# Performance work log

Hardware: AMD Instinct MI355X
Metric: run time of the kernel (lower is better)

Reference implementation:

```python
import jax, jax.numpy as jnp
import numpy as np

B, S, E, H = 8, 2048, 1024, 64

def setup_inputs() -> dict:
    key = jax.random.key(0)
    k1, k2, k3, k4 = jax.random.split(key, 4)
    scale = 0.02
    return {
        "x": jax.random.normal(k1, (B, S, E), dtype=jnp.float32),
        "Wq": jax.random.normal(k2, (E, H), dtype=jnp.float32) * scale,
        "Wk": jax.random.normal(k3, (E, H), dtype=jnp.float32) * scale,
        "Wv": jax.random.normal(k4, (E, H), dtype=jnp.float32) * scale,
    }

def reference(x, Wq, Wk, Wv):
    # x: [B, S, E]; projections to [B, S, H]
    q = jnp.einsum("bse,eh->bsh", x, Wq)
    k = jnp.einsum("bse,eh->bsh", x, Wk)
    v = jnp.einsum("bse,eh->bsh", x, Wv)
    head_size = Wq.shape[1]
    # NOTE: original divides by head_size (not sqrt(head_size))
    scores = jnp.einsum("bqh,bkh->bqk", q, k) / head_size  # [B, S, S]
    seq = q.shape[1]
    causal = jnp.tril(jnp.ones((seq, seq), dtype=bool))
    scores = jnp.where(causal, scores, -jnp.inf)
    attn = jax.nn.softmax(scores, axis=-1)
    # dropout p=0.0 (eval) -> identity
    return jnp.einsum("bqk,bkh->bqh", attn, v)
```

## Files before the change

kernel.cpp:

```cpp
#include <hip/hip_runtime.h>


typedef __bf16 bf16;
typedef bf16 bf16x8 __attribute__((ext_vector_type(8)));
typedef bf16 bf16x4 __attribute__((ext_vector_type(4)));
typedef float v4f __attribute__((ext_vector_type(4)));

#define MFMA_BF16 __builtin_amdgcn_mfma_f32_16x16x32_bf16

constexpr int SEQ = 2048, EDIM = 1024, HDIM = 64;
constexpr float SCALE_L2E = 1.4426950408889634f / 64.0f;

__global__ __launch_bounds__(256) void prep_w_kernel(
    const float* __restrict__ Wq, const float* __restrict__ Wk,
    const float* __restrict__ Wv, bf16* __restrict__ Wt) {
  int mat = blockIdx.x >> 5, kseg = blockIdx.x & 31;
  const float* src = mat == 0 ? Wq : (mat == 1 ? Wk : Wv);
  int n = threadIdx.x & 63;
  int k0 = kseg * 32 + (threadIdx.x >> 6) * 8;
  bf16x8 v;
#pragma unroll
  for (int j = 0; j < 8; ++j)
    v[j] = (bf16)src[(k0 + j) * 64 + n];
  *reinterpret_cast<bf16x8*>(Wt + (size_t)(mat * 64 + n) * EDIM + k0) = v;
}

__global__ __launch_bounds__(256) void proj_kernel(
    const float* __restrict__ x, const bf16* __restrict__ Wt,
    bf16* __restrict__ qw, bf16* __restrict__ kw, bf16* __restrict__ vT) {
  __shared__ __align__(16) bf16 As[2][32][72];
  __shared__ __align__(16) bf16 Bs[2][192][72];

  const int t = threadIdx.x;
  const int m0 = blockIdx.x * 32;
  const int wv = t >> 6, lane = t & 63, quad = lane >> 4, l16 = lane & 15;

  v4f acc[2][3] = {};
  float4 aReg[2];
  bf16x8 bReg[6];

  auto loadA = [&](int kk) {
#pragma unroll
    for (int p = 0; p < 2; ++p) {
      int flat = p * 1024 + t * 4;
      int r = flat >> 6, c = flat & 63;
      aReg[p] = *reinterpret_cast<const float4*>(
          x + (size_t)(m0 + r) * EDIM + kk * 64 + c);
    }
  };
  auto loadB = [&](int kk) {
#pragma unroll
    for (int p = 0; p < 6; ++p) {
      int idx = p * 256 + t;
      int r = idx >> 3, off = (idx & 7) * 8;
      bReg[p] = *reinterpret_cast<const bf16x8*>(
          Wt + (size_t)r * EDIM + kk * 64 + off);
    }
  };

  loadA(0);
  loadB(0);

  for (int kk = 0; kk < 16; ++kk) {
    const int buf = kk & 1;
#pragma unroll
    for (int p = 0; p < 2; ++p) {
      int flat = p * 1024 + t * 4;
      int r = flat >> 6, c = flat & 63;
      bf16x4 h4 = {(bf16)aReg[p].x, (bf16)aReg[p].y,
                   (bf16)aReg[p].z, (bf16)aReg[p].w};
      *reinterpret_cast<bf16x4*>(&As[buf][r][c]) = h4;
    }
#pragma unroll
    for (int p = 0; p < 6; ++p) {
      int idx = p * 256 + t;
      int r = idx >> 3, off = (idx & 7) * 8;
      *reinterpret_cast<bf16x8*>(&Bs[buf][r][off]) = bReg[p];
    }
    __syncthreads();
    if (kk < 15) {
      loadA(kk + 1);
      loadB(kk + 1);
    }
#pragma unroll
    for (int ks = 0; ks < 2; ++ks) {
      bf16x8 af[2], bfr[3];
#pragma unroll
      for (int mi = 0; mi < 2; ++mi)
        af[mi] = *reinterpret_cast<const bf16x8*>(
            &As[buf][16 * mi + l16][32 * ks + 8 * quad]);
#pragma unroll
      for (int ni = 0; ni < 3; ++ni)
        bfr[ni] = *reinterpret_cast<const bf16x8*>(
            &Bs[buf][48 * wv + 16 * ni + l16][32 * ks + 8 * quad]);
#pragma unroll
      for (int mi = 0; mi < 2; ++mi)
#pragma unroll
        for (int ni = 0; ni < 3; ++ni)
          acc[mi][ni] = MFMA_BF16(af[mi], bfr[ni], acc[mi][ni], 0, 0, 0);
    }
  }

#pragma unroll
  for (int mi = 0; mi < 2; ++mi) {
    const int token0 = m0 + 16 * mi + 4 * quad;
#pragma unroll
    for (int ni = 0; ni < 3; ++ni) {
      int n = 48 * wv + 16 * ni + l16;
      if (n < 64) {
#pragma unroll
        for (int r = 0; r < 4; ++r)
          qw[(size_t)(token0 + r) * HDIM + n] = (bf16)acc[mi][ni][r];
      } else if (n < 128) {
#pragma unroll
        for (int r = 0; r < 4; ++r)
          kw[(size_t)(token0 + r) * HDIM + (n - 64)] = (bf16)acc[mi][ni][r];
      } else {
        int b = token0 >> 11, s0 = token0 & 2047;
        bf16x4 pk = {(bf16)acc[mi][ni][0], (bf16)acc[mi][ni][1],
                     (bf16)acc[mi][ni][2], (bf16)acc[mi][ni][3]};
        *reinterpret_cast<bf16x4*>(
            vT + ((size_t)(b * 64 + (n - 128))) * SEQ + s0) = pk;
      }
    }
  }
}

__global__ __launch_bounds__(256) void attn_kernel(
    const bf16* __restrict__ qw, const bf16* __restrict__ kw,
    const bf16* __restrict__ vT, float* __restrict__ out) {
  const int batch = blockIdx.x & 7;
  const int j = blockIdx.x >> 3;
  const int w = threadIdx.x >> 6;
  const int lane = threadIdx.x & 63;
  const int quad = lane >> 4, l16 = lane & 15;

  __shared__ __align__(16) bf16 p_lds[4][16][40];
  __shared__ __align__(16) float o_lds[3][16][68];
  __shared__ float l_lds[3][16];

  const bf16* qB = qw + (size_t)batch * SEQ * HDIM;
  const bf16* kB = kw + (size_t)batch * SEQ * HDIM;
  const bf16* vB = vT + (size_t)batch * HDIM * SEQ;

  const int q0 = j * 16;
  const int T = (j >> 1) + 1;

  const bf16* qp = qB + (size_t)(q0 + l16) * HDIM + quad * 8;
  bf16x8 aq0 = *reinterpret_cast<const bf16x8*>(qp);
  bf16x8 aq1 = *reinterpret_cast<const bf16x8*>(qp + 32);

  float l_part[4] = {0.f, 0.f, 0.f, 0.f};
  v4f accO[4] = {};

  for (int jt = w; jt < T; jt += 4) {
    const int k0 = jt * 32;
    v4f sAcc[2] = {};
#pragma unroll
    for (int nt = 0; nt < 2; ++nt) {
      const bf16* kp = kB + (size_t)(k0 + 16 * nt + l16) * HDIM + quad * 8;
      bf16x8 b0 = *reinterpret_cast<const bf16x8*>(kp);
      bf16x8 b1 = *reinterpret_cast<const bf16x8*>(kp + 32);
      sAcc[nt] = MFMA_BF16(aq0, b0, sAcc[nt], 0, 0, 0);
      sAcc[nt] = MFMA_BF16(aq1, b1, sAcc[nt], 0, 0, 0);
    }
    float pv[2][4];
#pragma unroll
    for (int nt = 0; nt < 2; ++nt)
#pragma unroll
      for (int r = 0; r < 4; ++r)
        pv[nt][r] = __builtin_amdgcn_exp2f(sAcc[nt][r] * SCALE_L2E);
    if (jt == T - 1) {
#pragma unroll
      for (int nt = 0; nt < 2; ++nt)
#pragma unroll
        for (int r = 0; r < 4; ++r)
          if (k0 + 16 * nt + l16 > q0 + 4 * quad + r) pv[nt][r] = 0.f;
    }
#pragma unroll
    for (int r = 0; r < 4; ++r) l_part[r] += pv[0][r] + pv[1][r];

#pragma unroll
    for (int nt = 0; nt < 2; ++nt)
#pragma unroll
      for (int r = 0; r < 4; ++r)
        p_lds[w][4 * quad + r][16 * nt + l16] = (bf16)pv[nt][r];
    asm volatile("s_waitcnt lgkmcnt(0)" ::: "memory");
    bf16x8 pa = *reinterpret_cast<const bf16x8*>(&p_lds[w][l16][8 * quad]);
#pragma unroll
    for (int nt = 0; nt < 4; ++nt) {
      bf16x8 bv = *reinterpret_cast<const bf16x8*>(
          vB + (size_t)(16 * nt + l16) * SEQ + k0 + 8 * quad);
      accO[nt] = MFMA_BF16(pa, bv, accO[nt], 0, 0, 0);
    }
  }

#pragma unroll
  for (int r = 0; r < 4; ++r) {
    float s = l_part[r];
    s += __shfl_xor(s, 1, 16);
    s += __shfl_xor(s, 2, 16);
    s += __shfl_xor(s, 4, 16);
    s += __shfl_xor(s, 8, 16);
    l_part[r] = s;
  }

  if (w > 0) {
#pragma unroll
    for (int nt = 0; nt < 4; ++nt)
#pragma unroll
      for (int r = 0; r < 4; ++r)
        o_lds[w - 1][4 * quad + r][16 * nt + l16] = accO[nt][r];
    if (l16 == 0) {
#pragma unroll
      for (int r = 0; r < 4; ++r) l_lds[w - 1][4 * quad + r] = l_part[r];
    }
  }
  __syncthreads();
  if (w == 0) {
#pragma unroll
    for (int r = 0; r < 4; ++r) {
      const int row = 4 * quad + r;
      float lt = l_part[r] + l_lds[0][row] + l_lds[1][row] + l_lds[2][row];
      float inv = 1.0f / lt;
      float* op = out + ((size_t)batch * SEQ + q0 + row) * HDIM;
#pragma unroll
      for (int nt = 0; nt < 4; ++nt)
        op[16 * nt + l16] =
            (accO[nt][r] + o_lds[0][row][16 * nt + l16] +
             o_lds[1][row][16 * nt + l16] + o_lds[2][row][16 * nt + l16]) *
            inv;
    }
  }
}

extern "C" void kernel_launch(void* const* d_in, const int* in_sizes, int n_in,
                              void* d_out, int out_size, void* d_ws,
                              size_t ws_size, hipStream_t stream) {
  const float* x = (const float*)d_in[0];
  const float* Wq = (const float*)d_in[1];
  const float* Wk = (const float*)d_in[2];
  const float* Wv = (const float*)d_in[3];

  char* ws = (char*)d_ws;
  bf16* Wt = (bf16*)(ws);
  bf16* qw = (bf16*)(ws + 0x60000);
  bf16* kw = (bf16*)(ws + 0x260000);
  bf16* vT = (bf16*)(ws + 0x460000);

  prep_w_kernel<<<96, 256, 0, stream>>>(Wq, Wk, Wv, Wt);
  proj_kernel<<<512, 256, 0, stream>>>(x, Wt, qw, kw, vT);
  attn_kernel<<<1024, 256, 0, stream>>>(qw, kw, vT, (float*)d_out);
}
```

Baseline: 150.0 us.

## Enlarge attention tiles to 32x64, pair causal blocks, and software-pipeline QK with PV

The attention kernel now processes 32 query rows per tile against 64-key tiles, so each K and V fragment load feeds twice as many MFMAs. Each block handles a mirrored pair of query tiles (j and 63-j) to balance the causal triangle, and the grid shrinks from 1024 to 256 blocks. Within each wave, the next tile's K load and QK/exp stage overlap the current PV MFMAs through a double-buffered P buffer in LDS. The trade-off is larger register and LDS use and fewer blocks, which may reduce occupancy and latency hiding.

```diff
diff --git a/kernel.cpp b/kernel.cpp
--- a/kernel.cpp
+++ b/kernel.cpp
@@ -130,106 +130,153 @@
     const bf16* __restrict__ qw, const bf16* __restrict__ kw,
     const bf16* __restrict__ vT, float* __restrict__ out) {
   const int batch = blockIdx.x & 7;
-  const int j = blockIdx.x >> 3;
+  const int pi = blockIdx.x >> 3;
   const int w = threadIdx.x >> 6;
   const int lane = threadIdx.x & 63;
   const int quad = lane >> 4, l16 = lane & 15;
 
-  __shared__ __align__(16) bf16 p_lds[4][16][40];
-  __shared__ __align__(16) float o_lds[3][16][68];
-  __shared__ float l_lds[3][16];
+  __shared__ __align__(16) bf16 p_lds[4][2][32][68];
+  __shared__ __align__(16) float o_lds[3][32][68];
+  __shared__ float l_lds[3][32];
 
   const bf16* qB = qw + (size_t)batch * SEQ * HDIM;
   const bf16* kB = kw + (size_t)batch * SEQ * HDIM;
   const bf16* vB = vT + (size_t)batch * HDIM * SEQ;
 
-  const int q0 = j * 16;
-  const int T = (j >> 1) + 1;
-
-  const bf16* qp = qB + (size_t)(q0 + l16) * HDIM + quad * 8;
-  bf16x8 aq0 = *reinterpret_cast<const bf16x8*>(qp);
-  bf16x8 aq1 = *reinterpret_cast<const bf16x8*>(qp + 32);
-
-  float l_part[4] = {0.f, 0.f, 0.f, 0.f};
-  v4f accO[4] = {};
-
-  for (int jt = w; jt < T; jt += 4) {
-    const int k0 = jt * 32;
-    v4f sAcc[2] = {};
-#pragma unroll
-    for (int nt = 0; nt < 2; ++nt) {
-      const bf16* kp = kB + (size_t)(k0 + 16 * nt + l16) * HDIM + quad * 8;
-      bf16x8 b0 = *reinterpret_cast<const bf16x8*>(kp);
-      bf16x8 b1 = *reinterpret_cast<const bf16x8*>(kp + 32);
-      sAcc[nt] = MFMA_BF16(aq0, b0, sAcc[nt], 0, 0, 0);
-      sAcc[nt] = MFMA_BF16(aq1, b1, sAcc[nt], 0, 0, 0);
-    }
-    float pv[2][4];
-#pragma unroll
-    for (int nt = 0; nt < 2; ++nt)
-#pragma unroll
-      for (int r = 0; r < 4; ++r)
-        pv[nt][r] = __builtin_amdgcn_exp2f(sAcc[nt][r] * SCALE_L2E);
-    if (jt == T - 1) {
-#pragma unroll
-      for (int nt = 0; nt < 2; ++nt)
-#pragma unroll
-        for (int r = 0; r < 4; ++r)
-          if (k0 + 16 * nt + l16 > q0 + 4 * quad + r) pv[nt][r] = 0.f;
-    }
-#pragma unroll
-    for (int r = 0; r < 4; ++r) l_part[r] += pv[0][r] + pv[1][r];
-
-#pragma unroll
-    for (int nt = 0; nt < 2; ++nt)
-#pragma unroll
-      for (int r = 0; r < 4; ++r)
-        p_lds[w][4 * quad + r][16 * nt + l16] = (bf16)pv[nt][r];
-    asm volatile("s_waitcnt lgkmcnt(0)" ::: "memory");
-    bf16x8 pa = *reinterpret_cast<const bf16x8*>(&p_lds[w][l16][8 * quad]);
-#pragma unroll
-    for (int nt = 0; nt < 4; ++nt) {
-      bf16x8 bv = *reinterpret_cast<const bf16x8*>(
-          vB + (size_t)(16 * nt + l16) * SEQ + k0 + 8 * quad);
-      accO[nt] = MFMA_BF16(pa, bv, accO[nt], 0, 0, 0);
-    }
-  }
-
-#pragma unroll
-  for (int r = 0; r < 4; ++r) {
-    float s = l_part[r];
-    s += __shfl_xor(s, 1, 16);
-    s += __shfl_xor(s, 2, 16);
-    s += __shfl_xor(s, 4, 16);
-    s += __shfl_xor(s, 8, 16);
-    l_part[r] = s;
-  }
-
-  if (w > 0) {
-#pragma unroll
-    for (int nt = 0; nt < 4; ++nt)
-#pragma unroll
-      for (int r = 0; r < 4; ++r)
-        o_lds[w - 1][4 * quad + r][16 * nt + l16] = accO[nt][r];
-    if (l16 == 0) {
-#pragma unroll
-      for (int r = 0; r < 4; ++r) l_lds[w - 1][4 * quad + r] = l_part[r];
-    }
-  }
-  __syncthreads();
-  if (w == 0) {
-#pragma unroll
-    for (int r = 0; r < 4; ++r) {
-      const int row = 4 * quad + r;
-      float lt = l_part[r] + l_lds[0][row] + l_lds[1][row] + l_lds[2][row];
-      float inv = 1.0f / lt;
-      float* op = out + ((size_t)batch * SEQ + q0 + row) * HDIM;
+  for (int sp = 0; sp < 2; ++sp) {
+    const int j = sp ? (63 - pi) : pi;
+    const int q0 = 32 * j;
+    const int T64 = (j + 2) >> 1;
+    const int nw = (T64 > w) ? (((T64 - 1 - w) >> 2) + 1) : 0;
+
+    bf16x8 aq[2][2];
+#pragma unroll
+    for (int mi = 0; mi < 2; ++mi)
+#pragma unroll
+      for (int kf = 0; kf < 2; ++kf)
+        aq[mi][kf] = *reinterpret_cast<const bf16x8*>(
+            qB + (size_t)(q0 + 16 * mi + l16) * HDIM + 32 * kf + 8 * quad);
+
+    v4f accO[2][4] = {};
+    float l_part[2][4] = {{0.f, 0.f, 0.f, 0.f}, {0.f, 0.f, 0.f, 0.f}};
+    bf16x8 kfr[4][2];
+
+    auto loadK = [&](int jt) {
 #pragma unroll
       for (int nt = 0; nt < 4; ++nt)
-        op[16 * nt + l16] =
-            (accO[nt][r] + o_lds[0][row][16 * nt + l16] +
-             o_lds[1][row][16 * nt + l16] + o_lds[2][row][16 * nt + l16]) *
-            inv;
+#pragma unroll
+        for (int kf = 0; kf < 2; ++kf)
+          kfr[nt][kf] = *reinterpret_cast<const bf16x8*>(
+              kB + (size_t)(64 * jt + 16 * nt + l16) * HDIM + 32 * kf +
+              8 * quad);
+    };
+    auto qk_exp_stage = [&](int jt, int slot) {
+      v4f s[2][4] = {};
+#pragma unroll
+      for (int mi = 0; mi < 2; ++mi)
+#pragma unroll
+        for (int nt = 0; nt < 4; ++nt) {
+          s[mi][nt] = MFMA_BF16(aq[mi][0], kfr[nt][0], s[mi][nt], 0, 0, 0);
+          s[mi][nt] = MFMA_BF16(aq[mi][1], kfr[nt][1], s[mi][nt], 0, 0, 0);
+        }
+      const bool last = (jt == T64 - 1);
+#pragma unroll
+      for (int mi = 0; mi < 2; ++mi)
+#pragma unroll
+        for (int nt = 0; nt < 4; ++nt)
+#pragma unroll
+          for (int r = 0; r < 4; ++r) {
+            float p = __builtin_amdgcn_exp2f(s[mi][nt][r] * SCALE_L2E);
+            if (last &&
+                (64 * jt + 16 * nt + l16 > q0 + 16 * mi + 4 * quad + r))
+              p = 0.f;
+            l_part[mi][r] += p;
+            p_lds[w][slot][16 * mi + 4 * quad + r][16 * nt + l16] = (bf16)p;
+          }
+    };
+
+    if (nw > 0) {
+      loadK(w);
+      qk_exp_stage(w, 0);
+    }
+    for (int i = 0; i < nw; ++i) {
+      const int jt = w + 4 * i;
+      const int k0 = 64 * jt;
+      if (i + 1 < nw) loadK(jt + 4);
+      bf16x8 vfr[4][2];
+#pragma unroll
+      for (int nt = 0; nt < 4; ++nt)
+#pragma unroll
+        for (int kc = 0; kc < 2; ++kc)
+          vfr[nt][kc] = *reinterpret_cast<const bf16x8*>(
+              vB + (size_t)(16 * nt + l16) * SEQ + k0 + 32 * kc + 8 * quad);
+      asm volatile("s_waitcnt lgkmcnt(0)" ::: "memory");
+      bf16x8 pa[2][2];
+#pragma unroll
+      for (int mi = 0; mi < 2; ++mi)
+#pragma unroll
+        for (int kc = 0; kc < 2; ++kc)
+          pa[mi][kc] = *reinterpret_cast<const bf16x8*>(
+              &p_lds[w][i & 1][16 * mi + l16][32 * kc + 8 * quad]);
+      if (i + 1 < nw) qk_exp_stage(jt + 4, (i + 1) & 1);
+#pragma unroll
+      for (int mi = 0; mi < 2; ++mi)
+#pragma unroll
+        for (int nt = 0; nt < 4; ++nt) {
+          accO[mi][nt] = MFMA_BF16(pa[mi][0], vfr[nt][0], accO[mi][nt], 0, 0, 0);
+          accO[mi][nt] = MFMA_BF16(pa[mi][1], vfr[nt][1], accO[mi][nt], 0, 0, 0);
+        }
+    }
+
+#pragma unroll
+    for (int mi = 0; mi < 2; ++mi)
+#pragma unroll
+      for (int r = 0; r < 4; ++r) {
+        float s = l_part[mi][r];
+        s += __shfl_xor(s, 1, 16);
+        s += __shfl_xor(s, 2, 16);
+        s += __shfl_xor(s, 4, 16);
+        s += __shfl_xor(s, 8, 16);
+        l_part[mi][r] = s;
+      }
+
+    __syncthreads();
+    if (w > 0) {
+#pragma unroll
+      for (int mi = 0; mi < 2; ++mi)
+#pragma unroll
+        for (int nt = 0; nt < 4; ++nt)
+#pragma unroll
+          for (int r = 0; r < 4; ++r)
+            o_lds[w - 1][16 * mi + 4 * quad + r][16 * nt + l16] =
+                accO[mi][nt][r];
+      if (l16 == 0) {
+#pragma unroll
+        for (int mi = 0; mi < 2; ++mi)
+#pragma unroll
+          for (int r = 0; r < 4; ++r)
+            l_lds[w - 1][16 * mi + 4 * quad + r] = l_part[mi][r];
+      }
+    }
+    __syncthreads();
+    if (w == 0) {
+#pragma unroll
+      for (int mi = 0; mi < 2; ++mi)
+#pragma unroll
+        for (int r = 0; r < 4; ++r) {
+          const int row = 16 * mi + 4 * quad + r;
+          float lt = l_part[mi][r] + l_lds[0][row] + l_lds[1][row] +
+                     l_lds[2][row];
+          float inv = 1.0f / lt;
+          float* op = out + ((size_t)batch * SEQ + q0 + row) * HDIM;
+#pragma unroll
+          for (int nt = 0; nt < 4; ++nt)
+            op[16 * nt + l16] =
+                (accO[mi][nt][r] + o_lds[0][row][16 * nt + l16] +
+                 o_lds[1][row][16 * nt + l16] +
+                 o_lds[2][row][16 * nt + l16]) *
+                inv;
+        }
     }
   }
 }
@@ -250,5 +297,5 @@
 
   prep_w_kernel<<<96, 256, 0, stream>>>(Wq, Wk, Wv, Wt);
   proj_kernel<<<512, 256, 0, stream>>>(x, Wt, qw, kw, vT);
-  attn_kernel<<<1024, 256, 0, stream>>>(qw, kw, vT, (float*)d_out);
+  attn_kernel<<<256, 256, 0, stream>>>(qw, kw, vT, (float*)d_out);
 }
```

After: 136.4 us. 9.1% less time.

## Pipeline projection and attention loads, pair causal query tiles per block

Applied to the files above, without the earlier changes.

The projection kernel stops staging W in shared memory. Each wave now loads its W fragments straight into registers, double-buffered, and A is prefetched two steps ahead. The attention kernel processes 64-key tiles with software-pipelined K loads and QK/exp overlapped with PV, and each block handles a short and a long causal query tile (j and 127-j) to balance work across half as many blocks. This aims to hide global memory latency and even out causal load imbalance, at the cost of more registers and an added barrier per iteration.

```diff
diff --git a/kernel.cpp b/kernel.cpp
--- a/kernel.cpp
+++ b/kernel.cpp
@@ -29,76 +29,67 @@
     const float* __restrict__ x, const bf16* __restrict__ Wt,
     bf16* __restrict__ qw, bf16* __restrict__ kw, bf16* __restrict__ vT) {
   __shared__ __align__(16) bf16 As[2][32][72];
-  __shared__ __align__(16) bf16 Bs[2][192][72];
 
   const int t = threadIdx.x;
   const int m0 = blockIdx.x * 32;
   const int wv = t >> 6, lane = t & 63, quad = lane >> 4, l16 = lane & 15;
+  const int ar = t >> 3, ac = (t & 7) * 8;
 
   v4f acc[2][3] = {};
-  float4 aReg[2];
-  bf16x8 bReg[6];
-
-  auto loadA = [&](int kk) {
-#pragma unroll
-    for (int p = 0; p < 2; ++p) {
-      int flat = p * 1024 + t * 4;
-      int r = flat >> 6, c = flat & 63;
-      aReg[p] = *reinterpret_cast<const float4*>(
-          x + (size_t)(m0 + r) * EDIM + kk * 64 + c);
-    }
+  float4 aReg[2][2];
+  bf16x8 bReg[2][6];
+
+  auto loadA = [&](int kk, int slot) {
+    const float* p = x + (size_t)(m0 + ar) * EDIM + kk * 64 + ac;
+    aReg[slot][0] = *reinterpret_cast<const float4*>(p);
+    aReg[slot][1] = *reinterpret_cast<const float4*>(p + 4);
   };
-  auto loadB = [&](int kk) {
-#pragma unroll
-    for (int p = 0; p < 6; ++p) {
-      int idx = p * 256 + t;
-      int r = idx >> 3, off = (idx & 7) * 8;
-      bReg[p] = *reinterpret_cast<const bf16x8*>(
-          Wt + (size_t)r * EDIM + kk * 64 + off);
-    }
+  auto loadB = [&](int kk, int slot) {
+#pragma unroll
+    for (int ks = 0; ks < 2; ++ks)
+#pragma unroll
+      for (int ni = 0; ni < 3; ++ni)
+        bReg[slot][ks * 3 + ni] = *reinterpret_cast<const bf16x8*>(
+            Wt + (size_t)(48 * wv + 16 * ni + l16) * EDIM + kk * 64 +
+            32 * ks + 8 * quad);
   };
 
-  loadA(0);
-  loadB(0);
-
+  loadA(0, 0);
+  loadA(1, 1);
+  loadB(0, 0);
+
+#pragma unroll 2
   for (int kk = 0; kk < 16; ++kk) {
     const int buf = kk & 1;
-#pragma unroll
-    for (int p = 0; p < 2; ++p) {
-      int flat = p * 1024 + t * 4;
-      int r = flat >> 6, c = flat & 63;
-      bf16x4 h4 = {(bf16)aReg[p].x, (bf16)aReg[p].y,
-                   (bf16)aReg[p].z, (bf16)aReg[p].w};
-      *reinterpret_cast<bf16x4*>(&As[buf][r][c]) = h4;
-    }
-#pragma unroll
-    for (int p = 0; p < 6; ++p) {
-      int idx = p * 256 + t;
-      int r = idx >> 3, off = (idx & 7) * 8;
-      *reinterpret_cast<bf16x8*>(&Bs[buf][r][off]) = bReg[p];
-    }
-    __syncthreads();
-    if (kk < 15) {
-      loadA(kk + 1);
-      loadB(kk + 1);
-    }
-#pragma unroll
-    for (int ks = 0; ks < 2; ++ks) {
-      bf16x8 af[2], bfr[3];
+    {
+      bf16x8 h8;
+#pragma unroll
+      for (int e = 0; e < 4; ++e) {
+        h8[e] = (bf16)(&aReg[buf][0].x)[e];
+        h8[4 + e] = (bf16)(&aReg[buf][1].x)[e];
+      }
+      *reinterpret_cast<bf16x8*>(&As[buf][ar][ac]) = h8;
+    }
+    __syncthreads();
+    if (kk + 2 < 16) loadA(kk + 2, buf);
+    if (kk + 1 < 16) loadB(kk + 1, buf ^ 1);
+
+    bf16x8 af[2][2];
+#pragma unroll
+    for (int mi = 0; mi < 2; ++mi)
+#pragma unroll
+      for (int ks = 0; ks < 2; ++ks)
+        af[mi][ks] = *reinterpret_cast<const bf16x8*>(
+            &As[buf][16 * mi + l16][32 * ks + 8 * quad]);
+#pragma unroll
+    for (int ks = 0; ks < 2; ++ks)
 #pragma unroll
       for (int mi = 0; mi < 2; ++mi)
-        af[mi] = *reinterpret_cast<const bf16x8*>(
-            &As[buf][16 * mi + l16][32 * ks + 8 * quad]);
-#pragma unroll
-      for (int ni = 0; ni < 3; ++ni)
-        bfr[ni] = *reinterpret_cast<const bf16x8*>(
-            &Bs[buf][48 * wv + 16 * ni + l16][32 * ks + 8 * quad]);
-#pragma unroll
-      for (int mi = 0; mi < 2; ++mi)
 #pragma unroll
         for (int ni = 0; ni < 3; ++ni)
-          acc[mi][ni] = MFMA_BF16(af[mi], bfr[ni], acc[mi][ni], 0, 0, 0);
-    }
+          acc[mi][ni] =
+              MFMA_BF16(af[mi][ks], bReg[buf][ks * 3 + ni], acc[mi][ni], 0, 0, 0);
+    __syncthreads();
   }
 
 #pragma unroll
@@ -130,12 +121,12 @@
     const bf16* __restrict__ qw, const bf16* __restrict__ kw,
     const bf16* __restrict__ vT, float* __restrict__ out) {
   const int batch = blockIdx.x & 7;
-  const int j = blockIdx.x >> 3;
+  const int pi = blockIdx.x >> 3;
   const int w = threadIdx.x >> 6;
   const int lane = threadIdx.x & 63;
   const int quad = lane >> 4, l16 = lane & 15;
 
-  __shared__ __align__(16) bf16 p_lds[4][16][40];
+  __shared__ __align__(16) bf16 p_lds[4][2][16][68];
   __shared__ __align__(16) float o_lds[3][16][68];
   __shared__ float l_lds[3][16];
 
@@ -143,93 +134,118 @@
   const bf16* kB = kw + (size_t)batch * SEQ * HDIM;
   const bf16* vB = vT + (size_t)batch * HDIM * SEQ;
 
-  const int q0 = j * 16;
-  const int T = (j >> 1) + 1;
-
-  const bf16* qp = qB + (size_t)(q0 + l16) * HDIM + quad * 8;
-  bf16x8 aq0 = *reinterpret_cast<const bf16x8*>(qp);
-  bf16x8 aq1 = *reinterpret_cast<const bf16x8*>(qp + 32);
-
-  float l_part[4] = {0.f, 0.f, 0.f, 0.f};
-  v4f accO[4] = {};
-
-  for (int jt = w; jt < T; jt += 4) {
-    const int k0 = jt * 32;
-    v4f sAcc[2] = {};
-#pragma unroll
-    for (int nt = 0; nt < 2; ++nt) {
-      const bf16* kp = kB + (size_t)(k0 + 16 * nt + l16) * HDIM + quad * 8;
-      bf16x8 b0 = *reinterpret_cast<const bf16x8*>(kp);
-      bf16x8 b1 = *reinterpret_cast<const bf16x8*>(kp + 32);
-      sAcc[nt] = MFMA_BF16(aq0, b0, sAcc[nt], 0, 0, 0);
-      sAcc[nt] = MFMA_BF16(aq1, b1, sAcc[nt], 0, 0, 0);
-    }
-    float pv[2][4];
-#pragma unroll
-    for (int nt = 0; nt < 2; ++nt)
-#pragma unroll
-      for (int r = 0; r < 4; ++r)
-        pv[nt][r] = __builtin_amdgcn_exp2f(sAcc[nt][r] * SCALE_L2E);
-    if (jt == T - 1) {
-#pragma unroll
-      for (int nt = 0; nt < 2; ++nt)
+  for (int sp = 0; sp < 2; ++sp) {
+    const int j = sp ? (127 - pi) : pi;
+    const int q0 = 16 * j;
+    const int T64 = (j + 4) >> 2;
+    const int nw = (T64 > w) ? (((T64 - 1 - w) >> 2) + 1) : 0;
+
+    bf16x8 aq[2];
+#pragma unroll
+    for (int kf = 0; kf < 2; ++kf)
+      aq[kf] = *reinterpret_cast<const bf16x8*>(
+          qB + (size_t)(q0 + l16) * HDIM + 32 * kf + 8 * quad);
+
+    v4f accO[4] = {};
+    float l_part[4] = {0.f, 0.f, 0.f, 0.f};
+    bf16x8 kfr[2][4][2];
+
+    auto loadK = [&](int jt, int slot) {
+#pragma unroll
+      for (int nt = 0; nt < 4; ++nt)
+#pragma unroll
+        for (int kf = 0; kf < 2; ++kf)
+          kfr[slot][nt][kf] = *reinterpret_cast<const bf16x8*>(
+              kB + (size_t)(64 * jt + 16 * nt + l16) * HDIM + 32 * kf +
+              8 * quad);
+    };
+    auto qk_exp_stage = [&](int jt, int kslot, int pslot) {
+      v4f s[4] = {};
+#pragma unroll
+      for (int nt = 0; nt < 4; ++nt) {
+        s[nt] = MFMA_BF16(aq[0], kfr[kslot][nt][0], s[nt], 0, 0, 0);
+        s[nt] = MFMA_BF16(aq[1], kfr[kslot][nt][1], s[nt], 0, 0, 0);
+      }
+      const bool last = (jt == T64 - 1);
+#pragma unroll
+      for (int nt = 0; nt < 4; ++nt)
+#pragma unroll
+        for (int r = 0; r < 4; ++r) {
+          float p = __builtin_amdgcn_exp2f(s[nt][r] * SCALE_L2E);
+          if (last && (64 * jt + 16 * nt + l16 > q0 + 4 * quad + r)) p = 0.f;
+          l_part[r] += p;
+          p_lds[w][pslot][4 * quad + r][16 * nt + l16] = (bf16)p;
+        }
+    };
+
+    if (nw > 0) {
+      loadK(w, 0);
+      if (nw > 1) loadK(w + 4, 1);
+      qk_exp_stage(w, 0, 0);
+    }
+    for (int i = 0; i < nw; ++i) {
+      const int jt = w + 4 * i;
+      if (i + 2 < nw) loadK(jt + 8, i & 1);
+      bf16x8 vfr[4][2];
+#pragma unroll
+      for (int nt = 0; nt < 4; ++nt)
+#pragma unroll
+        for (int kc = 0; kc < 2; ++kc)
+          vfr[nt][kc] = *reinterpret_cast<const bf16x8*>(
+              vB + (size_t)(16 * nt + l16) * SEQ + 64 * jt + 32 * kc +
+              8 * quad);
+      asm volatile("s_waitcnt lgkmcnt(0)" ::: "memory");
+      bf16x8 pa[2];
+#pragma unroll
+      for (int kc = 0; kc < 2; ++kc)
+        pa[kc] = *reinterpret_cast<const bf16x8*>(
+            &p_lds[w][i & 1][l16][32 * kc + 8 * quad]);
+      if (i + 1 < nw) qk_exp_stage(jt + 4, (i + 1) & 1, (i + 1) & 1);
+#pragma unroll
+      for (int nt = 0; nt < 4; ++nt) {
+        accO[nt] = MFMA_BF16(pa[0], vfr[nt][0], accO[nt], 0, 0, 0);
+        accO[nt] = MFMA_BF16(pa[1], vfr[nt][1], accO[nt], 0, 0, 0);
+      }
+    }
+
+#pragma unroll
+    for (int r = 0; r < 4; ++r) {
+      float s = l_part[r];
+      s += __shfl_xor(s, 1, 16);
+      s += __shfl_xor(s, 2, 16);
+      s += __shfl_xor(s, 4, 16);
+      s += __shfl_xor(s, 8, 16);
+      l_part[r] = s;
+    }
+
+    __syncthreads();
+    if (w > 0) {
+#pragma unroll
+      for (int nt = 0; nt < 4; ++nt)
 #pragma unroll
         for (int r = 0; r < 4; ++r)
-          if (k0 + 16 * nt + l16 > q0 + 4 * quad + r) pv[nt][r] = 0.f;
-    }
-#pragma unroll
-    for (int r = 0; r < 4; ++r) l_part[r] += pv[0][r] + pv[1][r];
-
-#pragma unroll
-    for (int nt = 0; nt < 2; ++nt)
-#pragma unroll
-      for (int r = 0; r < 4; ++r)
-        p_lds[w][4 * quad + r][16 * nt + l16] = (bf16)pv[nt][r];
-    asm volatile("s_waitcnt lgkmcnt(0)" ::: "memory");
-    bf16x8 pa = *reinterpret_cast<const bf16x8*>(&p_lds[w][l16][8 * quad]);
-#pragma unroll
-    for (int nt = 0; nt < 4; ++nt) {
-      bf16x8 bv = *reinterpret_cast<const bf16x8*>(
-          vB + (size_t)(16 * nt + l16) * SEQ + k0 + 8 * quad);
-      accO[nt] = MFMA_BF16(pa, bv, accO[nt], 0, 0, 0);
-    }
-  }
-
-#pragma unroll
-  for (int r = 0; r < 4; ++r) {
-    float s = l_part[r];
-    s += __shfl_xor(s, 1, 16);
-    s += __shfl_xor(s, 2, 16);
-    s += __shfl_xor(s, 4, 16);
-    s += __shfl_xor(s, 8, 16);
-    l_part[r] = s;
-  }
-
-  if (w > 0) {
-#pragma unroll
-    for (int nt = 0; nt < 4; ++nt)
-#pragma unroll
-      for (int r = 0; r < 4; ++r)
-        o_lds[w - 1][4 * quad + r][16 * nt + l16] = accO[nt][r];
-    if (l16 == 0) {
-#pragma unroll
-      for (int r = 0; r < 4; ++r) l_lds[w - 1][4 * quad + r] = l_part[r];
-    }
-  }
-  __syncthreads();
-  if (w == 0) {
-#pragma unroll
-    for (int r = 0; r < 4; ++r) {
-      const int row = 4 * quad + r;
-      float lt = l_part[r] + l_lds[0][row] + l_lds[1][row] + l_lds[2][row];
-      float inv = 1.0f / lt;
-      float* op = out + ((size_t)batch * SEQ + q0 + row) * HDIM;
-#pragma unroll
-      for (int nt = 0; nt < 4; ++nt)
-        op[16 * nt + l16] =
-            (accO[nt][r] + o_lds[0][row][16 * nt + l16] +
-             o_lds[1][row][16 * nt + l16] + o_lds[2][row][16 * nt + l16]) *
-            inv;
+          o_lds[w - 1][4 * quad + r][16 * nt + l16] = accO[nt][r];
+      if (l16 == 0) {
+#pragma unroll
+        for (int r = 0; r < 4; ++r) l_lds[w - 1][4 * quad + r] = l_part[r];
+      }
+    }
+    __syncthreads();
+    if (w == 0) {
+#pragma unroll
+      for (int r = 0; r < 4; ++r) {
+        const int row = 4 * quad + r;
+        float lt =
+            l_part[r] + l_lds[0][row] + l_lds[1][row] + l_lds[2][row];
+        float inv = 1.0f / lt;
+        float* op = out + ((size_t)batch * SEQ + q0 + row) * HDIM;
+#pragma unroll
+        for (int nt = 0; nt < 4; ++nt)
+          op[16 * nt + l16] =
+              (accO[nt][r] + o_lds[0][row][16 * nt + l16] +
+               o_lds[1][row][16 * nt + l16] + o_lds[2][row][16 * nt + l16]) *
+              inv;
+      }
     }
   }
 }
@@ -250,5 +266,5 @@
 
   prep_w_kernel<<<96, 256, 0, stream>>>(Wq, Wk, Wv, Wt);
   proj_kernel<<<512, 256, 0, stream>>>(x, Wt, qw, kw, vT);
-  attn_kernel<<<1024, 256, 0, stream>>>(qw, kw, vT, (float*)d_out);
-}
+  attn_kernel<<<512, 256, 0, stream>>>(qw, kw, vT, (float*)d_out);
+}
```

Result: slower. 177.5 us (+18.3%).
